# Kernel tuning notes

Hardware: AMD Instinct MI355X
Metric: run time of the kernel (lower is better)

The kernel has to match this reference:

```python
import jax, jax.numpy as jnp
import numpy as np

H, C, HID, NLAYERS, B = 4, 32, 128, 3, 2048
EPS = 1e-5


def _gat_layer(x, src, dst, n, W, b, a_src, a_dst):
    # x: [N, HID]; W: [HID, H*C]; a_src/a_dst: [H, C]
    h = (x @ W).reshape(n, H, C)                      # [N,H,C]
    s_src = jnp.einsum('nhc,hc->nh', h, a_src)        # [N,H]
    s_dst = jnp.einsum('nhc,hc->nh', h, a_dst)
    e = jax.nn.leaky_relu(s_src[src] + s_dst[dst], 0.2)   # [E,H]
    m = jax.ops.segment_max(e, dst, num_segments=n)
    p = jnp.exp(e - m[dst])
    z = jax.ops.segment_sum(p, dst, num_segments=n)
    alpha = p / z[dst]                                 # scatter-softmax over in-edges
    msg = h[src] * alpha[:, :, None]                   # [E,H,C]
    out = jax.ops.segment_sum(msg, dst, num_segments=n)
    return out.reshape(n, H * C) + b


def _layernorm(x, g, bta):
    mu = jnp.mean(x, axis=-1, keepdims=True)
    var = jnp.mean(jnp.square(x - mu), axis=-1, keepdims=True)
    return (x - mu) * jax.lax.rsqrt(var + EPS) * g + bta


def _encode(x, edge_index, batch, W_in, b_in, Wg, bg, att_src, att_dst, ln_gamma, ln_beta):
    n = x.shape[0]
    # add self loops (PyG GATConv default)
    loops = jnp.arange(n, dtype=edge_index.dtype)
    src = jnp.concatenate([edge_index[0], loops])
    dst = jnp.concatenate([edge_index[1], loops])
    h = jax.nn.relu(x @ W_in + b_in)
    for i in range(NLAYERS):
        res = h
        h = _gat_layer(h, src, dst, n, Wg[i], bg[i], att_src[i], att_dst[i])
        h = _layernorm(h, ln_gamma[i], ln_beta[i])
        h = jax.nn.relu(h)
        h = h + res
    # global mean pool
    sums = jax.ops.segment_sum(h, batch, num_segments=B)
    cnt = jax.ops.segment_sum(jnp.ones((n,), h.dtype), batch, num_segments=B)
    return sums / jnp.maximum(cnt, 1.0)[:, None]


def setup_inputs() -> dict:
    key = jax.random.key(0)
    ks = jax.random.split(key, 24)
    Nt, Et, Np, Ep, D = 131072, 2097152, 24576, 196608, 480
    inp = {}
    inp['tcr_x'] = jax.random.normal(ks[0], (Nt, D), jnp.float32)
    inp['tcr_edge_index'] = jax.random.randint(ks[1], (2, Et), 0, Nt)
    inp['tcr_batch'] = jnp.sort(jax.random.randint(ks[2], (Nt,), 0, B))
    inp['pep_x'] = jax.random.normal(ks[3], (Np, D), jnp.float32)
    inp['pep_edge_index'] = jax.random.randint(ks[4], (2, Ep), 0, Np)
    inp['pep_batch'] = jnp.sort(jax.random.randint(ks[5], (Np,), 0, B))
    s_in = 1.0 / np.sqrt(D)
    inp['W_in'] = jax.random.normal(ks[6], (D, HID), jnp.float32) * s_in
    inp['b_in'] = jnp.zeros((HID,), jnp.float32)
    s_h = 1.0 / np.sqrt(HID)
    inp['Wg'] = jax.random.normal(ks[7], (NLAYERS, HID, H * C), jnp.float32) * s_h
    inp['bg'] = jnp.zeros((NLAYERS, HID), jnp.float32)
    inp['att_src'] = jax.random.normal(ks[8], (NLAYERS, H, C), jnp.float32) * (1.0 / np.sqrt(C))
    inp['att_dst'] = jax.random.normal(ks[9], (NLAYERS, H, C), jnp.float32) * (1.0 / np.sqrt(C))
    inp['ln_gamma'] = jnp.ones((NLAYERS, HID), jnp.float32)
    inp['ln_beta'] = jnp.zeros((NLAYERS, HID), jnp.float32)
    inp['Wc1'] = jax.random.normal(ks[10], (2 * HID, HID), jnp.float32) * (1.0 / np.sqrt(2 * HID))
    inp['bc1'] = jnp.zeros((HID,), jnp.float32)
    inp['Wc2'] = jax.random.normal(ks[11], (HID, HID // 2), jnp.float32) * s_h
    inp['bc2'] = jnp.zeros((HID // 2,), jnp.float32)
    inp['Wc3'] = jax.random.normal(ks[12], (HID // 2, 1), jnp.float32) * (1.0 / np.sqrt(HID // 2))
    inp['bc3'] = jnp.zeros((1,), jnp.float32)
    return inp


def reference(tcr_x, tcr_edge_index, tcr_batch, pep_x, pep_edge_index, pep_batch,
              W_in, b_in, Wg, bg, att_src, att_dst, ln_gamma, ln_beta,
              Wc1, bc1, Wc2, bc2, Wc3, bc3):
    tcr = _encode(tcr_x, tcr_edge_index, tcr_batch, W_in, b_in, Wg, bg, att_src, att_dst, ln_gamma, ln_beta)
    pep = _encode(pep_x, pep_edge_index, pep_batch, W_in, b_in, Wg, bg, att_src, att_dst, ln_gamma, ln_beta)
    z = jnp.concatenate([tcr, pep], axis=1)            # [B, 256]
    z = jax.nn.relu(z @ Wc1 + bc1)
    z = jax.nn.relu(z @ Wc2 + bc2)
    return jax.nn.sigmoid(z @ Wc3 + bc3)               # [B, 1]
```

## Files before the change

### kernel.cpp

```cpp
#include <hip/hip_runtime.h>
#include <hip/hip_fp16.h>
#include <math.h>

#define NHEAD   4
#define CDIM    32
#define HIDDIM  128
#define NLAYERS 3
#define DIN     480
#define LN_EPS  1e-5f
#define NSPLIT  4

typedef _Float16 f16x8 __attribute__((ext_vector_type(8)));
typedef float    f32x4 __attribute__((ext_vector_type(4)));

__global__ void hist_kernel(const int* __restrict__ tei, const int* __restrict__ pei,
                            int* __restrict__ deg, int Et, int Ep, int Nt, int N) {
    int i = blockIdx.x * 256 + threadIdx.x;
    int tot = Et + Ep + N;
    if (i >= tot) return;
    int d;
    if (i < Et)            d = tei[Et + i];
    else if (i < Et + Ep)  d = pei[Ep + (i - Et)] + Nt;
    else                   d = i - Et - Ep;
    atomicAdd(&deg[d], 1);
}

__global__ __launch_bounds__(256) void fill_kernel(const int* __restrict__ tei,
                                                   const int* __restrict__ pei,
                                                   int* __restrict__ cursor,
                                                   int* __restrict__ col,
                                                   int Et, int Ep, int Nt, int N,
                                                   float oscale) {
    int oid    = blockIdx.x & (NSPLIT - 1);
    int chunk  = blockIdx.x / NSPLIT;
    int nchunk = gridDim.x / NSPLIT;
    int tot = Et + Ep + N;
    int per = (tot + nchunk - 1) / nchunk;
    int e0 = chunk * per;
    int e1 = min(e0 + per, tot);
    for (int i = e0 + (int)threadIdx.x; i < e1; i += 256) {
        int d;
        bool self = false;
        if (i < Et)           d = tei[Et + i];
        else if (i < Et + Ep) d = pei[Ep + (i - Et)] + Nt;
        else                { d = i - Et - Ep; self = true; }
        int owner = (int)((float)d * oscale);
        owner = owner > NSPLIT - 1 ? NSPLIT - 1 : owner;
        if (owner != oid) continue;
        int s;
        if (self)        s = d;
        else if (i < Et) s = tei[i];
        else             s = pei[i - Et] + Nt;
        int pos = atomicAdd(&cursor[d], 1);
        col[pos] = s;
    }
}

__global__ __launch_bounds__(256) void scan_reduce(const int* __restrict__ deg,
                                                   int* __restrict__ part, int N) {
    __shared__ int sm[256];
    int t = threadIdx.x;
    int base = blockIdx.x * 1024 + t * 4;
    int4 v = make_int4(0, 0, 0, 0);
    if (base + 3 < N) v = *(const int4*)(deg + base);
    else if (base < N) {
        v.x = deg[base];
        if (base + 1 < N) v.y = deg[base + 1];
        if (base + 2 < N) v.z = deg[base + 2];
    }
    sm[t] = v.x + v.y + v.z + v.w;
    __syncthreads();
    for (int off = 128; off >= 1; off >>= 1) {
        if (t < off) sm[t] += sm[t + off];
        __syncthreads();
    }
    if (t == 0) part[blockIdx.x] = sm[0];
}

__global__ __launch_bounds__(256) void scan_partials(int* __restrict__ part,
                                                     int* __restrict__ rowptr,
                                                     int npart, int N) {
    __shared__ int sm[256];
    int t = threadIdx.x;
    sm[t] = (t < npart) ? part[t] : 0;
    __syncthreads();
    for (int off = 1; off < 256; off <<= 1) {
        int u = (t >= off) ? sm[t - off] : 0;
        __syncthreads();
        sm[t] += u;
        __syncthreads();
    }
    if (t < npart) part[t] = (t == 0) ? 0 : sm[t - 1];
    if (t == 0) rowptr[N] = sm[255];
}

__global__ __launch_bounds__(256) void scan_final(const int* __restrict__ deg,
                                                  const int* __restrict__ part,
                                                  int* __restrict__ rowptr,
                                                  int* __restrict__ cursor, int N) {
    __shared__ int sm[256];
    int t = threadIdx.x;
    int base = blockIdx.x * 1024 + t * 4;
    int4 v = make_int4(0, 0, 0, 0);
    if (base + 3 < N) v = *(const int4*)(deg + base);
    else if (base < N) {
        v.x = deg[base];
        if (base + 1 < N) v.y = deg[base + 1];
        if (base + 2 < N) v.z = deg[base + 2];
    }
    sm[t] = v.x + v.y + v.z + v.w;
    __syncthreads();
    for (int off = 1; off < 256; off <<= 1) {
        int u = (t >= off) ? sm[t - off] : 0;
        __syncthreads();
        sm[t] += u;
        __syncthreads();
    }
    int run = ((t == 0) ? 0 : sm[t - 1]) + part[blockIdx.x];
    if (base < N)     { rowptr[base]     = run; cursor[base]     = run; run += v.x; }
    if (base + 1 < N) { rowptr[base + 1] = run; cursor[base + 1] = run; run += v.y; }
    if (base + 2 < N) { rowptr[base + 2] = run; cursor[base + 2] = run; run += v.z; }
    if (base + 3 < N) { rowptr[base + 3] = run; cursor[base + 3] = run; }
}

__global__ void transpose_w(const float* __restrict__ W, _Float16* __restrict__ Wt,
                            int K) {
    int idx = blockIdx.x * 256 + threadIdx.x;
    if (idx >= K * 128) return;
    int n = idx / K, k = idx - n * K;
    Wt[idx] = (_Float16)W[(size_t)k * 128 + n];
}

#define ASTRIDE 40

template<int OUT_F16>
__global__ __launch_bounds__(256) void mfma_gemm(const float* __restrict__ A,
                                                 const _Float16* __restrict__ Wt,
                                                 const float* __restrict__ bias,
                                                 void* __restrict__ Cout,
                                                 int K) {
    __shared__ _Float16 As[64 * ASTRIDE];
    __shared__ _Float16 Ws[128 * ASTRIDE];
    const int tid  = threadIdx.x;
    const int bn   = blockIdx.x * 64;
    const int wave = tid >> 6, lane = tid & 63;
    const int lm   = lane & 15, q = lane >> 4;

    f32x4 acc[8];
#pragma unroll
    for (int i = 0; i < 8; ++i) acc[i] = (f32x4){0.f, 0.f, 0.f, 0.f};

    for (int kt = 0; kt < K; kt += 32) {
#pragma unroll
        for (int p = 0; p < 2; ++p) {
            int f  = p * 256 + tid;
            int r  = f >> 3;
            int c4 = (f & 7) * 4;
            float4 v = *(const float4*)(A + (size_t)(bn + r) * K + kt + c4);
            _Float16* d = &As[r * ASTRIDE + c4];
            d[0] = (_Float16)v.x; d[1] = (_Float16)v.y;
            d[2] = (_Float16)v.z; d[3] = (_Float16)v.w;
        }
#pragma unroll
        for (int p = 0; p < 2; ++p) {
            int f   = p * 256 + tid;
            int n   = f >> 2;
            int seg = (f & 3) * 8;
            *(float4*)(&Ws[n * ASTRIDE + seg]) =
                *(const float4*)(Wt + (size_t)n * K + kt + seg);
        }
        __syncthreads();
        f16x8 af = *(const f16x8*)(&As[(wave * 16 + lm) * ASTRIDE + q * 8]);
#pragma unroll
        for (int nt = 0; nt < 8; ++nt) {
            f16x8 bf = *(const f16x8*)(&Ws[(nt * 16 + lm) * ASTRIDE + q * 8]);
            acc[nt] = __builtin_amdgcn_mfma_f32_16x16x32_f16(af, bf, acc[nt], 0, 0, 0);
        }
        __syncthreads();
    }

    const int row0 = bn + wave * 16 + q * 4;
    if (OUT_F16) {
        _Float16* C = (_Float16*)Cout;
#pragma unroll
        for (int nt = 0; nt < 8; ++nt) {
            int c = nt * 16 + lm;
#pragma unroll
            for (int i = 0; i < 4; ++i)
                C[(size_t)(row0 + i) * 128 + c] = (_Float16)acc[nt][i];
        }
    } else {
        float* C = (float*)Cout;
#pragma unroll
        for (int nt = 0; nt < 8; ++nt) {
            int c = nt * 16 + lm;
            float bv = bias[c];
#pragma unroll
            for (int i = 0; i < 4; ++i)
                C[(size_t)(row0 + i) * 128 + c] = fmaxf(acc[nt][i] + bv, 0.f);
        }
    }
}

__global__ __launch_bounds__(256) void scores_kernel(const __half2* __restrict__ h2v,
                                                     const float* __restrict__ a_src,
                                                     const float* __restrict__ a_dst,
                                                     float* __restrict__ ssrc,
                                                     float* __restrict__ sdst, int N) {
    int wave = threadIdx.x >> 6, lane = threadIdx.x & 63;
    int n = blockIdx.x * 4 + wave;
    if (n >= N) return;
    int c = lane * 2, h = lane >> 4, t = lane & 15;
    float2 v = __half22float2(h2v[(size_t)n * 64 + lane]);
    float2 as = *(const float2*)(a_src + c);
    float2 ad = *(const float2*)(a_dst + c);
    float ps = v.x * as.x + v.y * as.y;
    float pd = v.x * ad.x + v.y * ad.y;
#pragma unroll
    for (int k = 1; k < 16; k <<= 1) {
        ps += __shfl_xor(ps, k, 16);
        pd += __shfl_xor(pd, k, 16);
    }
    if (t == 0) {
        ssrc[n * 4 + h] = ps;
        sdst[n * 4 + h] = pd;
    }
}

__global__ __launch_bounds__(256) void gather_kernel(const __half2* __restrict__ h2v,
                                                     const float* __restrict__ ssrc,
                                                     const float* __restrict__ sdst,
                                                     const int* __restrict__ rowptr,
                                                     const int* __restrict__ col,
                                                     const float* __restrict__ bg,
                                                     const float* __restrict__ gamma,
                                                     const float* __restrict__ beta,
                                                     float* __restrict__ hio, int N) {
    int wave = threadIdx.x >> 6, lane = threadIdx.x & 63;
    int n = blockIdx.x * 4 + wave;
    if (n >= N) return;
    int c = lane * 2, h = lane >> 4;
    int beg = rowptr[n], end = rowptr[n + 1];
    float sd = sdst[n * 4 + h];
    float m = -1e30f, z = 0.f, a0 = 0.f, a1 = 0.f;
    int j = beg;
    for (; j + 3 < end; j += 4) {
        int s0 = col[j], s1 = col[j + 1], s2 = col[j + 2], s3 = col[j + 3];
        float e0 = ssrc[s0 * 4 + h] + sd;
        float e1 = ssrc[s1 * 4 + h] + sd;
        float e2 = ssrc[s2 * 4 + h] + sd;
        float e3 = ssrc[s3 * 4 + h] + sd;
        float2 v0 = __half22float2(h2v[(size_t)s0 * 64 + lane]);
        float2 v1 = __half22float2(h2v[(size_t)s1 * 64 + lane]);
        float2 v2 = __half22float2(h2v[(size_t)s2 * 64 + lane]);
        float2 v3 = __half22float2(h2v[(size_t)s3 * 64 + lane]);
        e0 = e0 > 0.f ? e0 : 0.2f * e0;
        e1 = e1 > 0.f ? e1 : 0.2f * e1;
        e2 = e2 > 0.f ? e2 : 0.2f * e2;
        e3 = e3 > 0.f ? e3 : 0.2f * e3;
        float nm = fmaxf(fmaxf(fmaxf(e0, e1), fmaxf(e2, e3)), m);
        float r  = __expf(m - nm);
        m = nm;
        float p0 = __expf(e0 - nm);
        float p1 = __expf(e1 - nm);
        float p2 = __expf(e2 - nm);
        float p3 = __expf(e3 - nm);
        a0 *= r; a1 *= r; z *= r;
        a0 = fmaf(p0, v0.x, a0); a1 = fmaf(p0, v0.y, a1);
        a0 = fmaf(p1, v1.x, a0); a1 = fmaf(p1, v1.y, a1);
        a0 = fmaf(p2, v2.x, a0); a1 = fmaf(p2, v2.y, a1);
        a0 = fmaf(p3, v3.x, a0); a1 = fmaf(p3, v3.y, a1);
        z += p0 + p1 + p2 + p3;
    }
    for (; j < end; ++j) {
        int s = col[j];
        float e = ssrc[s * 4 + h] + sd;
        e = e > 0.f ? e : 0.2f * e;
        float2 v = __half22float2(h2v[(size_t)s * 64 + lane]);
        float nm = fmaxf(m, e);
        float r  = __expf(m - nm);
        float p  = __expf(e - nm);
        m = nm;
        a0 = fmaf(p, v.x, a0 * r);
        a1 = fmaf(p, v.y, a1 * r);
        z  = z * r + p;
    }
    float inv = 1.f / z;
    float2 bgv = *(const float2*)(bg + c);
    float o0 = a0 * inv + bgv.x;
    float o1 = a1 * inv + bgv.y;
    float s = o0 + o1;
#pragma unroll
    for (int k = 1; k < 64; k <<= 1) s += __shfl_xor(s, k);
    float mu = s * (1.f / 128.f);
    float q = (o0 - mu) * (o0 - mu) + (o1 - mu) * (o1 - mu);
#pragma unroll
    for (int k = 1; k < 64; k <<= 1) q += __shfl_xor(q, k);
    float rs = rsqrtf(q * (1.f / 128.f) + LN_EPS);
    float2 gm = *(const float2*)(gamma + c);
    float2 bt = *(const float2*)(beta + c);
    float y0 = (o0 - mu) * rs * gm.x + bt.x;
    float y1 = (o1 - mu) * rs * gm.y + bt.y;
    float2 r = *(const float2*)(hio + (size_t)n * 128 + c);
    y0 = fmaxf(y0, 0.f) + r.x;
    y1 = fmaxf(y1, 0.f) + r.y;
    *(float2*)(hio + (size_t)n * 128 + c) = make_float2(y0, y1);
}

__global__ __launch_bounds__(256) void pool_kernel(const float* __restrict__ h,
                                                   const int* __restrict__ tb,
                                                   const int* __restrict__ pb,
                                                   float* __restrict__ pooled,
                                                   int* __restrict__ cnt,
                                                   int Nt, int N, int B) {
    int wave = threadIdx.x >> 6, lane = threadIdx.x & 63;
    int n = blockIdx.x * 4 + wave;
    if (n >= N) return;
    int b, off, ci;
    if (n < Nt) { b = tb[n];      off = 0;   ci = b; }
    else        { b = pb[n - Nt]; off = 128; ci = B + b; }
    float v0 = h[(size_t)n * 128 + lane];
    float v1 = h[(size_t)n * 128 + 64 + lane];
    atomicAdd(&pooled[(size_t)b * 256 + off + lane], v0);
    atomicAdd(&pooled[(size_t)b * 256 + off + 64 + lane], v1);
    if (lane == 0) atomicAdd(&cnt[ci], 1);
}

__global__ __launch_bounds__(128) void classifier_kernel(const float* __restrict__ pooled,
                                                         const int* __restrict__ cnt,
                                                         const float* __restrict__ Wc1,
                                                         const float* __restrict__ bc1,
                                                         const float* __restrict__ Wc2,
                                                         const float* __restrict__ bc2,
                                                         const float* __restrict__ Wc3,
                                                         const float* __restrict__ bc3,
                                                         float* __restrict__ outp, int B) {
    __shared__ float z[256];
    __shared__ float a1[128];
    __shared__ float a2[64];
    int r = blockIdx.x, t = threadIdx.x;
    float ct = (float)max(cnt[r], 1);
    float cp = (float)max(cnt[B + r], 1);
    z[t]       = pooled[(size_t)r * 256 + t] / ct;
    z[128 + t] = pooled[(size_t)r * 256 + 128 + t] / cp;
    __syncthreads();
    float acc = bc1[t];
    for (int k = 0; k < 256; ++k) acc = fmaf(z[k], Wc1[k * 128 + t], acc);
    a1[t] = fmaxf(acc, 0.f);
    __syncthreads();
    if (t < 64) {
        float a = bc2[t];
        for (int k = 0; k < 128; ++k) a = fmaf(a1[k], Wc2[k * 64 + t], a);
        a2[t] = fmaxf(a, 0.f);
    }
    __syncthreads();
    if (t < 64) {
        float p = a2[t] * Wc3[t];
#pragma unroll
        for (int k = 1; k < 64; k <<= 1) p += __shfl_xor(p, k);
        if (t == 0) outp[r] = 1.f / (1.f + __expf(-(p + bc3[0])));
    }
}

extern "C" void kernel_launch(void* const* d_in, const int* in_sizes, int n_in,
                              void* d_out, int out_size, void* d_ws, size_t ws_size,
                              hipStream_t stream) {
    const float* tcr_x     = (const float*)d_in[0];
    const int*   tcr_ei    = (const int*)d_in[1];
    const int*   tcr_batch = (const int*)d_in[2];
    const float* pep_x     = (const float*)d_in[3];
    const int*   pep_ei    = (const int*)d_in[4];
    const int*   pep_batch = (const int*)d_in[5];
    const float* W_in      = (const float*)d_in[6];
    const float* b_in      = (const float*)d_in[7];
    const float* Wg        = (const float*)d_in[8];
    const float* bg        = (const float*)d_in[9];
    const float* att_src   = (const float*)d_in[10];
    const float* att_dst   = (const float*)d_in[11];
    const float* ln_gamma  = (const float*)d_in[12];
    const float* ln_beta   = (const float*)d_in[13];
    const float* Wc1       = (const float*)d_in[14];
    const float* bc1       = (const float*)d_in[15];
    const float* Wc2       = (const float*)d_in[16];
    const float* bc2       = (const float*)d_in[17];
    const float* Wc3       = (const float*)d_in[18];
    const float* bc3       = (const float*)d_in[19];

    const int Nt = in_sizes[0] / DIN;
    const int Et = in_sizes[1] / 2;
    const int Np = in_sizes[3] / DIN;
    const int Ep = in_sizes[4] / 2;
    const int B  = out_size;
    const int N  = Nt + Np;
    const int Etot = Et + Ep + N;

    char* w = (char*)d_ws;
    size_t o = 0;
    auto alloc = [&](size_t bytes) -> char* {
        size_t r = (o + 255) & ~(size_t)255;
        o = r + bytes;
        return w + r;
    };
    float*    pooled = (float*)alloc((size_t)B * 256 * 4);
    int*      cnt    = (int*)alloc((size_t)B * 2 * 4);
    float*    h_a    = (float*)alloc((size_t)N * 128 * 4);
    _Float16* h2h    = (_Float16*)alloc((size_t)N * 128 * 2);
    _Float16* WtIn   = (_Float16*)alloc((size_t)128 * DIN * 2);
    _Float16* WtG    = (_Float16*)alloc((size_t)NLAYERS * 128 * 128 * 2);
    float*    ssrc   = (float*)alloc((size_t)N * 4 * 4);
    float*    sdst   = (float*)alloc((size_t)N * 4 * 4);
    int* rowptr      = (int*)alloc((size_t)(N + 1) * 4);
    int* cursor      = (int*)alloc((size_t)N * 4);
    int* deg         = (int*)alloc((size_t)N * 4);
    int* part        = (int*)alloc(256 * 4);
    int* col         = (int*)alloc((size_t)Etot * 4);
    (void)ws_size; (void)n_in;

    hipMemsetAsync(pooled, 0, (size_t)B * 256 * 4, stream);
    hipMemsetAsync(cnt, 0, (size_t)B * 2 * 4, stream);
    hipMemsetAsync(deg, 0, (size_t)N * 4, stream);

    transpose_w<<<(128 * DIN + 255) / 256, 256, 0, stream>>>(W_in, WtIn, DIN);
    for (int i = 0; i < NLAYERS; ++i)
        transpose_w<<<(128 * 128 + 255) / 256, 256, 0, stream>>>(
            Wg + (size_t)i * HIDDIM * HIDDIM, WtG + (size_t)i * 128 * 128, 128);

    hist_kernel<<<(Etot + 255) / 256, 256, 0, stream>>>(tcr_ei, pep_ei, deg, Et, Ep, Nt, N);
    int nblk = (N + 1023) / 1024;
    scan_reduce<<<nblk, 256, 0, stream>>>(deg, part, N);
    scan_partials<<<1, 256, 0, stream>>>(part, rowptr, nblk, N);
    scan_final<<<nblk, 256, 0, stream>>>(deg, part, rowptr, cursor, N);
    fill_kernel<<<NSPLIT * 512, 256, 0, stream>>>(tcr_ei, pep_ei, cursor, col,
                                                  Et, Ep, Nt, N, (float)NSPLIT / (float)N);

    mfma_gemm<0><<<Nt / 64, 256, 0, stream>>>(tcr_x, WtIn, b_in, h_a, DIN);
    mfma_gemm<0><<<Np / 64, 256, 0, stream>>>(pep_x, WtIn, b_in, h_a + (size_t)Nt * 128, DIN);

    for (int i = 0; i < NLAYERS; ++i) {
        mfma_gemm<1><<<N / 64, 256, 0, stream>>>(h_a, WtG + (size_t)i * 128 * 128,
                                                 nullptr, h2h, 128);
        scores_kernel<<<(N + 3) / 4, 256, 0, stream>>>((const __half2*)h2h,
                                                       att_src + i * NHEAD * CDIM,
                                                       att_dst + i * NHEAD * CDIM,
                                                       ssrc, sdst, N);
        gather_kernel<<<(N + 3) / 4, 256, 0, stream>>>((const __half2*)h2h, ssrc, sdst,
                                                       rowptr, col, bg + i * HIDDIM,
                                                       ln_gamma + i * HIDDIM,
                                                       ln_beta + i * HIDDIM, h_a, N);
    }
    pool_kernel<<<(N + 3) / 4, 256, 0, stream>>>(h_a, tcr_batch, pep_batch, pooled, cnt, Nt, N, B);

    classifier_kernel<<<B, 128, 0, stream>>>(pooled, cnt, Wc1, bc1, Wc2, bc2,
                                             Wc3, bc3, (float*)d_out, B);
}
```

Measured before the change: 1.361 ms.

## Process four nodes per wave in GAT gather with 16-byte feature loads

The GAT gather/softmax/LayerNorm kernel now gives each 16-lane group its own destination node, so a wave handles four nodes instead of one. Each lane loads 8 fp16 features (16 bytes) per neighbour instead of 2, and the four column indices per step come from one vector load. This raises memory-level parallelism and cuts per-edge instruction overhead in the dominant edge-gather loop. In exchange each lane holds more registers, and degree imbalance among the four nodes sharing a wave causes divergence.

Result: faster. 1.293 ms (-5.0%).

```diff
diff --git a/kernel.cpp b/kernel.cpp
--- a/kernel.cpp
+++ b/kernel.cpp
@@ -12,6 +12,7 @@
 
 typedef _Float16 f16x8 __attribute__((ext_vector_type(8)));
 typedef float    f32x4 __attribute__((ext_vector_type(4)));
+typedef int      int4u __attribute__((ext_vector_type(4), aligned(4)));
 
 __global__ void hist_kernel(const int* __restrict__ tei, const int* __restrict__ pei,
                             int* __restrict__ deg, int Et, int Ep, int Nt, int N) {
@@ -227,7 +228,7 @@
     }
 }
 
-__global__ __launch_bounds__(256) void gather_kernel(const __half2* __restrict__ h2v,
+__global__ __launch_bounds__(256) void gather_kernel(const f16x8* __restrict__ h2v,
                                                      const float* __restrict__ ssrc,
                                                      const float* __restrict__ sdst,
                                                      const int* __restrict__ rowptr,
@@ -237,27 +238,36 @@
                                                      const float* __restrict__ beta,
                                                      float* __restrict__ hio, int N) {
     int wave = threadIdx.x >> 6, lane = threadIdx.x & 63;
-    int n = blockIdx.x * 4 + wave;
-    if (n >= N) return;
-    int c = lane * 2, h = lane >> 4;
-    int beg = rowptr[n], end = rowptr[n + 1];
-    float sd = sdst[n * 4 + h];
-    float m = -1e30f, z = 0.f, a0 = 0.f, a1 = 0.f;
+    int g = lane >> 4, t = lane & 15;
+    int n = blockIdx.x * 16 + wave * 4 + g;
+    bool valid = n < N;
+    int nn = valid ? n : 0;
+    int head = t >> 2;
+    int beg = rowptr[nn];
+    int end = valid ? rowptr[nn + 1] : beg;
+    float sd = sdst[nn * 4 + head];
+
+    float m = -1e30f, z = 0.f;
+    float a[8];
+#pragma unroll
+    for (int k = 0; k < 8; ++k) a[k] = 0.f;
+
     int j = beg;
     for (; j + 3 < end; j += 4) {
-        int s0 = col[j], s1 = col[j + 1], s2 = col[j + 2], s3 = col[j + 3];
-        float e0 = ssrc[s0 * 4 + h] + sd;
-        float e1 = ssrc[s1 * 4 + h] + sd;
-        float e2 = ssrc[s2 * 4 + h] + sd;
-        float e3 = ssrc[s3 * 4 + h] + sd;
-        float2 v0 = __half22float2(h2v[(size_t)s0 * 64 + lane]);
-        float2 v1 = __half22float2(h2v[(size_t)s1 * 64 + lane]);
-        float2 v2 = __half22float2(h2v[(size_t)s2 * 64 + lane]);
-        float2 v3 = __half22float2(h2v[(size_t)s3 * 64 + lane]);
-        e0 = e0 > 0.f ? e0 : 0.2f * e0;
-        e1 = e1 > 0.f ? e1 : 0.2f * e1;
-        e2 = e2 > 0.f ? e2 : 0.2f * e2;
-        e3 = e3 > 0.f ? e3 : 0.2f * e3;
+        int4u cv = *(const int4u*)(col + j);
+        int s0 = cv.x, s1 = cv.y, s2 = cv.z, s3 = cv.w;
+        float e0 = ssrc[s0 * 4 + head] + sd;
+        float e1 = ssrc[s1 * 4 + head] + sd;
+        float e2 = ssrc[s2 * 4 + head] + sd;
+        float e3 = ssrc[s3 * 4 + head] + sd;
+        f16x8 v0 = h2v[(size_t)s0 * 16 + t];
+        f16x8 v1 = h2v[(size_t)s1 * 16 + t];
+        f16x8 v2 = h2v[(size_t)s2 * 16 + t];
+        f16x8 v3 = h2v[(size_t)s3 * 16 + t];
+        e0 = fmaxf(e0, 0.2f * e0);
+        e1 = fmaxf(e1, 0.2f * e1);
+        e2 = fmaxf(e2, 0.2f * e2);
+        e3 = fmaxf(e3, 0.2f * e3);
         float nm = fmaxf(fmaxf(fmaxf(e0, e1), fmaxf(e2, e3)), m);
         float r  = __expf(m - nm);
         m = nm;
@@ -265,46 +275,72 @@
         float p1 = __expf(e1 - nm);
         float p2 = __expf(e2 - nm);
         float p3 = __expf(e3 - nm);
-        a0 *= r; a1 *= r; z *= r;
-        a0 = fmaf(p0, v0.x, a0); a1 = fmaf(p0, v0.y, a1);
-        a0 = fmaf(p1, v1.x, a0); a1 = fmaf(p1, v1.y, a1);
-        a0 = fmaf(p2, v2.x, a0); a1 = fmaf(p2, v2.y, a1);
-        a0 = fmaf(p3, v3.x, a0); a1 = fmaf(p3, v3.y, a1);
-        z += p0 + p1 + p2 + p3;
+        z = z * r + (p0 + p1 + p2 + p3);
+#pragma unroll
+        for (int k = 0; k < 8; ++k) a[k] *= r;
+#pragma unroll
+        for (int k = 0; k < 8; ++k) a[k] = fmaf((float)v0[k], p0, a[k]);
+#pragma unroll
+        for (int k = 0; k < 8; ++k) a[k] = fmaf((float)v1[k], p1, a[k]);
+#pragma unroll
+        for (int k = 0; k < 8; ++k) a[k] = fmaf((float)v2[k], p2, a[k]);
+#pragma unroll
+        for (int k = 0; k < 8; ++k) a[k] = fmaf((float)v3[k], p3, a[k]);
     }
     for (; j < end; ++j) {
         int s = col[j];
-        float e = ssrc[s * 4 + h] + sd;
-        e = e > 0.f ? e : 0.2f * e;
-        float2 v = __half22float2(h2v[(size_t)s * 64 + lane]);
+        float e = ssrc[s * 4 + head] + sd;
+        e = fmaxf(e, 0.2f * e);
+        f16x8 v = h2v[(size_t)s * 16 + t];
         float nm = fmaxf(m, e);
         float r  = __expf(m - nm);
         float p  = __expf(e - nm);
         m = nm;
-        a0 = fmaf(p, v.x, a0 * r);
-        a1 = fmaf(p, v.y, a1 * r);
-        z  = z * r + p;
-    }
+        z = z * r + p;
+#pragma unroll
+        for (int k = 0; k < 8; ++k) a[k] = fmaf((float)v[k], p, a[k] * r);
+    }
+
+    if (!valid) return;
     float inv = 1.f / z;
-    float2 bgv = *(const float2*)(bg + c);
-    float o0 = a0 * inv + bgv.x;
-    float o1 = a1 * inv + bgv.y;
-    float s = o0 + o1;
-#pragma unroll
-    for (int k = 1; k < 64; k <<= 1) s += __shfl_xor(s, k);
+    int c0 = t * 8;
+    float4 bgv0 = *(const float4*)(bg + c0);
+    float4 bgv1 = *(const float4*)(bg + c0 + 4);
+    float o[8];
+    o[0] = a[0] * inv + bgv0.x; o[1] = a[1] * inv + bgv0.y;
+    o[2] = a[2] * inv + bgv0.z; o[3] = a[3] * inv + bgv0.w;
+    o[4] = a[4] * inv + bgv1.x; o[5] = a[5] * inv + bgv1.y;
+    o[6] = a[6] * inv + bgv1.z; o[7] = a[7] * inv + bgv1.w;
+    float s = 0.f;
+#pragma unroll
+    for (int k = 0; k < 8; ++k) s += o[k];
+#pragma unroll
+    for (int k = 1; k < 16; k <<= 1) s += __shfl_xor(s, k, 16);
     float mu = s * (1.f / 128.f);
-    float q = (o0 - mu) * (o0 - mu) + (o1 - mu) * (o1 - mu);
-#pragma unroll
-    for (int k = 1; k < 64; k <<= 1) q += __shfl_xor(q, k);
+    float q = 0.f;
+#pragma unroll
+    for (int k = 0; k < 8; ++k) q += (o[k] - mu) * (o[k] - mu);
+#pragma unroll
+    for (int k = 1; k < 16; k <<= 1) q += __shfl_xor(q, k, 16);
     float rs = rsqrtf(q * (1.f / 128.f) + LN_EPS);
-    float2 gm = *(const float2*)(gamma + c);
-    float2 bt = *(const float2*)(beta + c);
-    float y0 = (o0 - mu) * rs * gm.x + bt.x;
-    float y1 = (o1 - mu) * rs * gm.y + bt.y;
-    float2 r = *(const float2*)(hio + (size_t)n * 128 + c);
-    y0 = fmaxf(y0, 0.f) + r.x;
-    y1 = fmaxf(y1, 0.f) + r.y;
-    *(float2*)(hio + (size_t)n * 128 + c) = make_float2(y0, y1);
+    float4 gm0 = *(const float4*)(gamma + c0);
+    float4 gm1 = *(const float4*)(gamma + c0 + 4);
+    float4 bt0 = *(const float4*)(beta + c0);
+    float4 bt1 = *(const float4*)(beta + c0 + 4);
+    float* hrow = hio + (size_t)n * 128 + c0;
+    float4 r0 = *(const float4*)(hrow);
+    float4 r1 = *(const float4*)(hrow + 4);
+    float4 y0, y1;
+    y0.x = fmaxf((o[0] - mu) * rs * gm0.x + bt0.x, 0.f) + r0.x;
+    y0.y = fmaxf((o[1] - mu) * rs * gm0.y + bt0.y, 0.f) + r0.y;
+    y0.z = fmaxf((o[2] - mu) * rs * gm0.z + bt0.z, 0.f) + r0.z;
+    y0.w = fmaxf((o[3] - mu) * rs * gm0.w + bt0.w, 0.f) + r0.w;
+    y1.x = fmaxf((o[4] - mu) * rs * gm1.x + bt1.x, 0.f) + r1.x;
+    y1.y = fmaxf((o[5] - mu) * rs * gm1.y + bt1.y, 0.f) + r1.y;
+    y1.z = fmaxf((o[6] - mu) * rs * gm1.z + bt1.z, 0.f) + r1.z;
+    y1.w = fmaxf((o[7] - mu) * rs * gm1.w + bt1.w, 0.f) + r1.w;
+    *(float4*)(hrow)     = y0;
+    *(float4*)(hrow + 4) = y1;
 }
 
 __global__ __launch_bounds__(256) void pool_kernel(const float* __restrict__ h,
@@ -443,10 +479,10 @@
                                                        att_src + i * NHEAD * CDIM,
                                                        att_dst + i * NHEAD * CDIM,
                                                        ssrc, sdst, N);
-        gather_kernel<<<(N + 3) / 4, 256, 0, stream>>>((const __half2*)h2h, ssrc, sdst,
-                                                       rowptr, col, bg + i * HIDDIM,
-                                                       ln_gamma + i * HIDDIM,
-                                                       ln_beta + i * HIDDIM, h_a, N);
+        gather_kernel<<<(N + 15) / 16, 256, 0, stream>>>((const f16x8*)h2h, ssrc, sdst,
+                                                         rowptr, col, bg + i * HIDDIM,
+                                                         ln_gamma + i * HIDDIM,
+                                                         ln_beta + i * HIDDIM, h_a, N);
     }
     pool_kernel<<<(N + 3) / 4, 256, 0, stream>>>(h_a, tcr_batch, pep_batch, pooled, cnt, Nt, N, B);
 
```
